# Performance work log

Measured on AMD Instinct MI355X. Metric: run time of the kernel, lower is better.

## Reference

```python
import jax, jax.numpy as jnp
import numpy as np

VOCAB, BLOCK, C, H, L = 65, 60, 384, 6, 6
HS = C // H  # 64
EPS = 1e-5


def _ln(x, g, b):
    mu = jnp.mean(x, axis=-1, keepdims=True)
    var = jnp.mean(jnp.square(x - mu), axis=-1, keepdims=True)
    return (x - mu) * jax.lax.rsqrt(var + EPS) * g + b


def setup_inputs() -> dict:
    key = jax.random.key(0)
    ks = jax.random.split(key, 16)
    std = 0.02
    B, T = 2048, 60
    inp = {
        'context': jax.random.randint(ks[0], (B, T), 0, VOCAB),
        'tok_emb': std * jax.random.normal(ks[1], (VOCAB, C), jnp.float32),
        'pos_emb': std * jax.random.normal(ks[2], (BLOCK, C), jnp.float32),
        # per-head projections stacked: [L, H, C, HS]
        'wq': std * jax.random.normal(ks[3], (L, H, C, HS), jnp.float32),
        'wk': std * jax.random.normal(ks[4], (L, H, C, HS), jnp.float32),
        'wv': std * jax.random.normal(ks[5], (L, H, C, HS), jnp.float32),
        'wo': std * jax.random.normal(ks[6], (L, C, C), jnp.float32),
        'bo': jnp.zeros((L, C), jnp.float32),
        'ln1_g': jnp.ones((L, C), jnp.float32),
        'ln1_b': jnp.zeros((L, C), jnp.float32),
        'ln2_g': jnp.ones((L, C), jnp.float32),
        'ln2_b': jnp.zeros((L, C), jnp.float32),
        'w1': std * jax.random.normal(ks[7], (L, C, 4 * C), jnp.float32),
        'b1': jnp.zeros((L, 4 * C), jnp.float32),
        'w2': std * jax.random.normal(ks[8], (L, 4 * C, C), jnp.float32),
        'b2': jnp.zeros((L, C), jnp.float32),
        'lnf_g': jnp.ones((C,), jnp.float32),
        'lnf_b': jnp.zeros((C,), jnp.float32),
        'lm_w': std * jax.random.normal(ks[9], (C, VOCAB), jnp.float32),
        'lm_b': jnp.zeros((VOCAB,), jnp.float32),
    }
    return inp


def _forward(context, tok_emb, pos_emb, wq, wk, wv, wo, bo,
             ln1_g, ln1_b, ln2_g, ln2_b, w1, b1, w2, b2,
             lnf_g, lnf_b, lm_w, lm_b):
    B, T = context.shape
    x = tok_emb[context] + pos_emb[:T]  # [B,T,C]
    causal = jnp.tril(jnp.ones((T, T), bool))
    neg_inf = jnp.finfo(x.dtype).min

    def block(x, p):
        (wq_l, wk_l, wv_l, wo_l, bo_l, g1, b1n, g2, b2n, w1_l, bb1, w2_l, bb2) = p
        h = _ln(x, g1, b1n)
        q = jnp.einsum('btc,hcd->bhtd', h, wq_l)
        k = jnp.einsum('btc,hcd->bhtd', h, wk_l)
        v = jnp.einsum('btc,hcd->bhtd', h, wv_l)
        scores = jnp.einsum('bhtd,bhsd->bhts', q, k) * (HS ** -0.5)
        scores = jnp.where(causal, scores, neg_inf)
        probs = jax.nn.softmax(scores, axis=-1)
        o = jnp.einsum('bhts,bhsd->bhtd', probs, v)
        o = o.transpose(0, 2, 1, 3).reshape(B, T, C)  # concat heads
        x = x + o @ wo_l + bo_l
        h = _ln(x, g2, b2n)
        x = x + jax.nn.relu(h @ w1_l + bb1) @ w2_l + bb2
        return x, None

    params = (wq, wk, wv, wo, bo, ln1_g, ln1_b, ln2_g, ln2_b, w1, b1, w2, b2)
    x, _ = jax.lax.scan(block, x, params)
    x = _ln(x, lnf_g, lnf_b)
    return x @ lm_w + lm_b  # [B,T,VOCAB]


def reference(context, tok_emb, pos_emb, wq, wk, wv, wo, bo,
              ln1_g, ln1_b, ln2_g, ln2_b, w1, b1, w2, b2,
              lnf_g, lnf_b, lm_w, lm_b):
    return _forward(context, tok_emb, pos_emb, wq, wk, wv, wo, bo,
                    ln1_g, ln1_b, ln2_g, ln2_b, w1, b1, w2, b2,
                    lnf_g, lnf_b, lm_w, lm_b)
```

## Files before the change

### kernel.cpp

```cpp
#include <hip/hip_runtime.h>


#define B_  2048
#define T_  60
#define C_  384
#define H_  6
#define HS_ 64
#define L_  6
#define FF_ 1536
#define V_  65

typedef unsigned int  u32;
typedef unsigned short u16;
typedef short bf16x8 __attribute__((ext_vector_type(8)));
typedef float f32x4  __attribute__((ext_vector_type(4)));

__device__ __forceinline__ float bf2f(u32 u) {
  return __uint_as_float(u << 16);
}
__device__ __forceinline__ u16 f2bf(float f) {
  u32 u = __float_as_uint(f);
  u = u + 0x7FFFu + ((u >> 16) & 1u);
  return (u16)(u >> 16);
}

__global__ void tconv_k(const float* __restrict__ src, u16* __restrict__ dst,
                        int K, int N, long srcStride, int nH, long sL, long sH)
{
  __shared__ float t[32][33];
  int z = blockIdx.z;
  int l = z / nH, hh = z % nH;
  const float* s = src + (long)z * srcStride;
  u16* d = dst + l * sL + hh * sH;
  int n0 = blockIdx.x * 32, k0 = blockIdx.y * 32;
  for (int yy = threadIdx.y; yy < 32; yy += 8) {
    int k = k0 + yy, n = n0 + threadIdx.x;
    t[yy][threadIdx.x] = (k < K && n < N) ? s[(long)k * N + n] : 0.f;
  }
  __syncthreads();
  for (int yy = threadIdx.y; yy < 32; yy += 8) {
    int n = n0 + yy, k = k0 + threadIdx.x;
    if (n < N && k < K) d[(long)n * K + k] = f2bf(t[threadIdx.x][yy]);
  }
}

__global__ __launch_bounds__(256) void embed_k(const int* __restrict__ ctx,
    const float* __restrict__ tok, const float* __restrict__ pos,
    float* __restrict__ x)
{
  int idx = blockIdx.x * 256 + threadIdx.x;
  int row = idx / (C_ / 4);
  int c   = (idx % (C_ / 4)) * 4;
  int t   = row % T_;
  int tk  = ctx[row];
  float4 a = *(const float4*)(tok + (long)tk * C_ + c);
  float4 p = *(const float4*)(pos + (long)t  * C_ + c);
  float4 o = make_float4(a.x + p.x, a.y + p.y, a.z + p.z, a.w + p.w);
  *(float4*)(x + (long)idx * 4) = o;
}

__global__ __launch_bounds__(256) void ln_k(const float* __restrict__ x,
    const float* __restrict__ g, const float* __restrict__ b,
    u16* __restrict__ h)
{
  int lane = threadIdx.x & 63;
  int wv   = threadIdx.x >> 6;
  long row = (long)blockIdx.x * 4 + wv;
  const float* xr = x + row * C_;
  int c0 = lane * 6;
  float v0[6];
  #pragma unroll
  for (int i = 0; i < 6; i++) v0[i] = xr[c0 + i];
  float s = 0.f, sq = 0.f;
  #pragma unroll
  for (int i = 0; i < 6; i++) { s += v0[i]; sq += v0[i] * v0[i]; }
  #pragma unroll
  for (int off = 32; off > 0; off >>= 1) {
    s  += __shfl_xor(s,  off, 64);
    sq += __shfl_xor(sq, off, 64);
  }
  float mu  = s * (1.f / C_);
  float var = sq * (1.f / C_) - mu * mu;
  float rs  = rsqrtf(var + 1e-5f);
  u16* hr = h + row * C_;
  #pragma unroll
  for (int i = 0; i < 6; i++) {
    float hv = (v0[i] - mu) * rs * g[c0 + i] + b[c0 + i];
    hr[c0 + i] = f2bf(hv);
  }
}

template<int RELU, int RES, int OBF>
__global__ __launch_bounds__(256) void gemm128d(const u16* __restrict__ A,
    const u16* __restrict__ Wt, const float* __restrict__ bias,
    const float* __restrict__ resid, void* __restrict__ outp,
    int N, int K, int mT, int nT)
{
  __shared__ __align__(16) u16 As[2][4][128][8];
  __shared__ __align__(16) u16 Bs[2][4][128][8];
  int tid = threadIdx.x;
  int bid = blockIdx.x;
  int mtile, ntile;
  if ((mT & 7) == 0) {
    int xcd = bid & 7, loc = bid >> 3;
    int q = loc / nT;
    mtile = xcd * (mT >> 3) + q;
    ntile = loc - q * nT;
  } else {
    int q = bid / nT;
    mtile = q;
    ntile = bid - q * nT;
  }
  long mBase = (long)mtile * 128;
  int  nBase = ntile * 128;
  int lane = tid & 63, wv = tid >> 6;
  int l15 = lane & 15, l4 = lane >> 4;
  int sk = tid & 3, sr = tid >> 2;
  const u16* aP = A + (mBase + sr) * (long)K + sk * 8;
  const u16* bP = Wt + ((long)nBase + sr) * K + sk * 8;
  const long rStep = (long)64 * K;

  f32x4 acc[2][8];
  #pragma unroll
  for (int i = 0; i < 2; i++)
    #pragma unroll
    for (int j = 0; j < 8; j++)
      acc[i][j] = (f32x4){0.f, 0.f, 0.f, 0.f};

  uint4 ar0 = *(const uint4*)aP;
  uint4 ar1 = *(const uint4*)(aP + rStep);
  uint4 br0 = *(const uint4*)bP;
  uint4 br1 = *(const uint4*)(bP + rStep);
  *(uint4*)&As[0][sk][sr][0]      = ar0;
  *(uint4*)&As[0][sk][sr + 64][0] = ar1;
  *(uint4*)&Bs[0][sk][sr][0]      = br0;
  *(uint4*)&Bs[0][sk][sr + 64][0] = br1;
  if (K > 32) {
    ar0 = *(const uint4*)(aP + 32);
    ar1 = *(const uint4*)(aP + rStep + 32);
    br0 = *(const uint4*)(bP + 32);
    br1 = *(const uint4*)(bP + rStep + 32);
  }
  __syncthreads();

  int cur = 0;
  for (int k0 = 0; k0 < K; k0 += 32) {
    bf16x8 af[2], bfr[8];
    af[0] = *(const bf16x8*)&As[cur][l4][wv * 32 + l15][0];
    af[1] = *(const bf16x8*)&As[cur][l4][wv * 32 + 16 + l15][0];
    #pragma unroll
    for (int j = 0; j < 8; j++)
      bfr[j] = *(const bf16x8*)&Bs[cur][l4][j * 16 + l15][0];
    if (k0 + 32 < K) {
      int nb = cur ^ 1;
      *(uint4*)&As[nb][sk][sr][0]      = ar0;
      *(uint4*)&As[nb][sk][sr + 64][0] = ar1;
      *(uint4*)&Bs[nb][sk][sr][0]      = br0;
      *(uint4*)&Bs[nb][sk][sr + 64][0] = br1;
      if (k0 + 64 < K) {
        ar0 = *(const uint4*)(aP + k0 + 64);
        ar1 = *(const uint4*)(aP + rStep + k0 + 64);
        br0 = *(const uint4*)(bP + k0 + 64);
        br1 = *(const uint4*)(bP + rStep + k0 + 64);
      }
    }
    #pragma unroll
    for (int i = 0; i < 2; i++)
      #pragma unroll
      for (int j = 0; j < 8; j++)
        acc[i][j] = __builtin_amdgcn_mfma_f32_16x16x32_bf16(
            af[i], bfr[j], acc[i][j], 0, 0, 0);
    __syncthreads();
    cur ^= 1;
  }

  #pragma unroll
  for (int i = 0; i < 2; i++) {
    #pragma unroll
    for (int j = 0; j < 8; j++) {
      int n = nBase + j * 16 + l15;
      float bv = bias ? bias[n] : 0.f;
      #pragma unroll
      for (int r = 0; r < 4; r++) {
        long row = mBase + wv * 32 + i * 16 + l4 * 4 + r;
        float vv = acc[i][j][r] + bv;
        if (RELU) vv = fmaxf(vv, 0.f);
        if (RES)  vv += resid[row * N + n];
        if (OBF) ((u16*)outp)[row * N + n] = f2bf(vv);
        else     ((float*)outp)[row * N + n] = vv;
      }
    }
  }
}

template<int OBF>
__global__ __launch_bounds__(256) void gemm_head(const u16* __restrict__ A,
    const u16* __restrict__ Wt, const float* __restrict__ bias,
    void* __restrict__ outp, int N, int K)
{
  __shared__ __align__(16) u16 As[4][128][8];
  __shared__ __align__(16) u16 Bs[4][64][8];
  int tid  = threadIdx.x;
  int nt   = blockIdx.x;
  int nBase = nt * 64;
  long mBase = (long)blockIdx.y * 128;
  int lane = tid & 63, wv = tid >> 6;
  int l15 = lane & 15, l4 = lane >> 4;
  int sseg = tid & 3;
  int srow = tid >> 2;
  const u16* a0p = A + (mBase + srow) * K + sseg * 8;
  const u16* a1p = a0p + (long)64 * K;
  bool colOK = (nBase + srow) < N;
  const u16* bp  = Wt + (long)(nBase + srow) * K + sseg * 8;

  f32x4 acc[2][4];
  #pragma unroll
  for (int i = 0; i < 2; i++)
    #pragma unroll
    for (int j = 0; j < 4; j++)
      acc[i][j] = (f32x4){0.f, 0.f, 0.f, 0.f};

  for (int k0 = 0; k0 < K; k0 += 32) {
    uint4 av0 = *(const uint4*)(a0p + k0);
    uint4 av1 = *(const uint4*)(a1p + k0);
    uint4 bv  = colOK ? *(const uint4*)(bp + k0) : make_uint4(0, 0, 0, 0);
    *(uint4*)&As[sseg][srow][0]      = av0;
    *(uint4*)&As[sseg][srow + 64][0] = av1;
    *(uint4*)&Bs[sseg][srow][0]      = bv;
    __syncthreads();
    bf16x8 af[2], bfr[4];
    af[0] = *(const bf16x8*)&As[l4][wv * 32 + l15][0];
    af[1] = *(const bf16x8*)&As[l4][wv * 32 + 16 + l15][0];
    #pragma unroll
    for (int j = 0; j < 4; j++)
      bfr[j] = *(const bf16x8*)&Bs[l4][j * 16 + l15][0];
    #pragma unroll
    for (int i = 0; i < 2; i++)
      #pragma unroll
      for (int j = 0; j < 4; j++)
        acc[i][j] = __builtin_amdgcn_mfma_f32_16x16x32_bf16(
            af[i], bfr[j], acc[i][j], 0, 0, 0);
    __syncthreads();
  }

  #pragma unroll
  for (int i = 0; i < 2; i++) {
    #pragma unroll
    for (int j = 0; j < 4; j++) {
      int n = nBase + j * 16 + l15;
      if (n < N) {
        #pragma unroll
        for (int r = 0; r < 4; r++) {
          long row = mBase + wv * 32 + i * 16 + l4 * 4 + r;
          float vv = acc[i][j][r];
          if (bias) vv += bias[n];
          if (OBF) ((u16*)outp)[row * N + n] = f2bf(vv);
          else     ((float*)outp)[row * N + n] = vv;
        }
      }
    }
  }
}

__global__ __launch_bounds__(256) void attn_k(const u16* __restrict__ qkv,
    u16* __restrict__ ao)
{
  __shared__ __align__(16) u16 qs[64][72];
  __shared__ __align__(16) u16 ks[64][72];
  __shared__ __align__(16) u16 vT[64][72];
  __shared__ __align__(16) u16 ps[64][72];
  int tid = threadIdx.x;
  int bb = blockIdx.x / H_;
  int hh = blockIdx.x % H_;
  const u16* base = qkv + ((long)bb * T_) * 1152 + hh * HS_;

  for (int i = tid; i < 576; i += 256)
    ((uint4*)vT)[i] = make_uint4(0, 0, 0, 0);
  __syncthreads();

  for (int i = tid; i < 480; i += 256) {
    int t = i >> 3, d0 = (i & 7) << 3;
    const u16* rp = base + (long)t * 1152;
    *(uint4*)&qs[t][d0] = *(const uint4*)(rp + d0);
    *(uint4*)&ks[t][d0] = *(const uint4*)(rp + 384 + d0);
    uint4 rv = *(const uint4*)(rp + 768 + d0);
    u16 vv[8] = {(u16)(rv.x & 0xffffu), (u16)(rv.x >> 16),
                 (u16)(rv.y & 0xffffu), (u16)(rv.y >> 16),
                 (u16)(rv.z & 0xffffu), (u16)(rv.z >> 16),
                 (u16)(rv.w & 0xffffu), (u16)(rv.w >> 16)};
    #pragma unroll
    for (int m = 0; m < 8; m++) vT[d0 + m][t] = vv[m];
  }
  __syncthreads();

  int lane = tid & 63, wv = tid >> 6;
  int l15 = lane & 15, quad = lane >> 4;

  bf16x8 aq0 = *(const bf16x8*)&qs[wv * 16 + l15][quad * 8];
  bf16x8 aq1 = *(const bf16x8*)&qs[wv * 16 + l15][32 + quad * 8];
  f32x4 s[4];
  #pragma unroll
  for (int jt = 0; jt < 4; jt++) {
    bf16x8 b0 = *(const bf16x8*)&ks[jt * 16 + l15][quad * 8];
    bf16x8 b1 = *(const bf16x8*)&ks[jt * 16 + l15][32 + quad * 8];
    f32x4 a2 = (f32x4){0.f, 0.f, 0.f, 0.f};
    a2 = __builtin_amdgcn_mfma_f32_16x16x32_bf16(aq0, b0, a2, 0, 0, 0);
    a2 = __builtin_amdgcn_mfma_f32_16x16x32_bf16(aq1, b1, a2, 0, 0, 0);
    s[jt] = a2;
  }

  int rbase = wv * 16 + quad * 4;
  #pragma unroll
  for (int r = 0; r < 4; r++) {
    int row = rbase + r;
    float v0[4];
    #pragma unroll
    for (int jt = 0; jt < 4; jt++) {
      int col = jt * 16 + l15;
      float sv = s[jt][r] * 0.125f;
      v0[jt] = (col <= row) ? sv : -1e30f;
    }
    float m = fmaxf(fmaxf(v0[0], v0[1]), fmaxf(v0[2], v0[3]));
    #pragma unroll
    for (int off = 1; off < 16; off <<= 1) m = fmaxf(m, __shfl_xor(m, off, 64));
    float sum = 0.f;
    #pragma unroll
    for (int jt = 0; jt < 4; jt++) { v0[jt] = __expf(v0[jt] - m); sum += v0[jt]; }
    #pragma unroll
    for (int off = 1; off < 16; off <<= 1) sum += __shfl_xor(sum, off, 64);
    float inv = 1.f / sum;
    #pragma unroll
    for (int jt = 0; jt < 4; jt++)
      ps[row][jt * 16 + l15] = f2bf(v0[jt] * inv);
  }
  __syncthreads();

  bf16x8 ap0 = *(const bf16x8*)&ps[wv * 16 + l15][quad * 8];
  bf16x8 ap1 = *(const bf16x8*)&ps[wv * 16 + l15][32 + quad * 8];
  long obase = ((long)bb * T_) * C_ + hh * HS_;
  #pragma unroll
  for (int dt = 0; dt < 4; dt++) {
    bf16x8 b0 = *(const bf16x8*)&vT[dt * 16 + l15][quad * 8];
    bf16x8 b1 = *(const bf16x8*)&vT[dt * 16 + l15][32 + quad * 8];
    f32x4 a2 = (f32x4){0.f, 0.f, 0.f, 0.f};
    a2 = __builtin_amdgcn_mfma_f32_16x16x32_bf16(ap0, b0, a2, 0, 0, 0);
    a2 = __builtin_amdgcn_mfma_f32_16x16x32_bf16(ap1, b1, a2, 0, 0, 0);
    #pragma unroll
    for (int r = 0; r < 4; r++) {
      int row = rbase + r;
      if (row < T_)
        ao[obase + (long)row * C_ + dt * 16 + l15] = f2bf(a2[r]);
    }
  }
}

extern "C" void kernel_launch(void* const* d_in, const int* in_sizes, int n_in,
                              void* d_out, int out_size, void* d_ws, size_t ws_size,
                              hipStream_t stream)
{
  const int*   ctx  = (const int*)  d_in[0];
  const float* tok  = (const float*)d_in[1];
  const float* pos  = (const float*)d_in[2];
  const float* wq   = (const float*)d_in[3];
  const float* wk   = (const float*)d_in[4];
  const float* wv   = (const float*)d_in[5];
  const float* wo   = (const float*)d_in[6];
  const float* bo   = (const float*)d_in[7];
  const float* ln1g = (const float*)d_in[8];
  const float* ln1b = (const float*)d_in[9];
  const float* ln2g = (const float*)d_in[10];
  const float* ln2b = (const float*)d_in[11];
  const float* w1   = (const float*)d_in[12];
  const float* b1   = (const float*)d_in[13];
  const float* w2   = (const float*)d_in[14];
  const float* b2   = (const float*)d_in[15];
  const float* lnfg = (const float*)d_in[16];
  const float* lnfb = (const float*)d_in[17];
  const float* lmw  = (const float*)d_in[18];
  const float* lmb  = (const float*)d_in[19];
  float* out = (float*)d_out;

  const long nQKV = (long)L_ * H_ * C_ * HS_;
  const long nWO  = (long)L_ * C_ * C_;
  const long nW1  = (long)L_ * C_ * FF_;
  const long nLM  = (long)C_ * V_;
  u16* wqkvT = (u16*)d_ws;
  u16* woT = wqkvT + 3 * nQKV;
  u16* w1T = woT + nWO;
  u16* w2T = w1T + nW1;
  u16* lmT = w2T + nW1;
  const size_t wbytes = (size_t)(nQKV * 3 + nWO + nW1 * 2 + nLM) * 2;

  int chunkB = 32;
  {
    const int cand[] = {2048, 1024, 512, 256, 128, 64, 32};
    for (int i = 0; i < 7; i++) {
      size_t U = (size_t)cand[i] * T_ * C_ * 2;
      if (wbytes + 7 * U <= ws_size) { chunkB = cand[i]; break; }
    }
  }
  const long BTc = (long)chunkB * T_;
  char* wsb = (char*)d_ws + wbytes;
  const size_t U = (size_t)BTc * C_ * 2;
  float* x    = (float*)wsb;
  u16*   h    = (u16*)(wsb + 2 * U);
  char*  reg  = wsb + 3 * U;
  u16* qkvb = (u16*)reg;
  u16* ab   = (u16*)(reg + 3 * U);
  u16* fb   = (u16*)reg;

  {
    dim3 tb(32, 8);
    const long sL = 1152L * 384, sH = 64L * 384, sec = 384L * 384;
    tconv_k<<<dim3(2, 12, L_ * H_), tb, 0, stream>>>(wq, wqkvT,
        C_, HS_, (long)C_ * HS_, H_, sL, sH);
    tconv_k<<<dim3(2, 12, L_ * H_), tb, 0, stream>>>(wk, wqkvT + sec,
        C_, HS_, (long)C_ * HS_, H_, sL, sH);
    tconv_k<<<dim3(2, 12, L_ * H_), tb, 0, stream>>>(wv, wqkvT + 2 * sec,
        C_, HS_, (long)C_ * HS_, H_, sL, sH);
    tconv_k<<<dim3(12, 12, L_), tb, 0, stream>>>(wo, woT,
        C_, C_, (long)C_ * C_, 1, (long)C_ * C_, 0);
    tconv_k<<<dim3(48, 12, L_), tb, 0, stream>>>(w1, w1T,
        C_, FF_, (long)C_ * FF_, 1, (long)C_ * FF_, 0);
    tconv_k<<<dim3(12, 48, L_), tb, 0, stream>>>(w2, w2T,
        FF_, C_, (long)FF_ * C_, 1, (long)FF_ * C_, 0);
    tconv_k<<<dim3(3, 12, 1), tb, 0, stream>>>(lmw, lmT,
        C_, V_, (long)C_ * V_, 1, 0, 0);
  }

  const long qkvL = 1152L * 384;
  const long woL  = (long)C_ * C_;
  const long w1L  = (long)C_ * FF_;
  dim3 blk(256);
  dim3 gEmb((u32)(BTc * C_ / 4 / 256));
  dim3 gLN((u32)(BTc / 4));
  int mT = (int)(BTc / 128);
  dim3 gHd(2, (u32)(BTc / 128));
  dim3 gAt((u32)(chunkB * H_));

  for (int c0 = 0; c0 < B_; c0 += chunkB) {
    const long tok0 = (long)c0 * T_;
    const int* ctxc = ctx + tok0;
    float* outc = out + tok0 * V_;

    embed_k<<<gEmb, blk, 0, stream>>>(ctxc, tok, pos, x);

    for (int l = 0; l < L_; l++) {
      ln_k<<<gLN, blk, 0, stream>>>(x, ln1g + l * C_, ln1b + l * C_, h);
      gemm128d<0,0,1><<<dim3(mT * 9), blk, 0, stream>>>(h, wqkvT + l * qkvL,
          nullptr, nullptr, qkvb, 1152, C_, mT, 9);
      attn_k<<<gAt, blk, 0, stream>>>(qkvb, ab);
      gemm128d<0,1,0><<<dim3(mT * 3), blk, 0, stream>>>(ab, woT + l * woL,
          bo + l * C_, x, x, C_, C_, mT, 3);
      ln_k<<<gLN, blk, 0, stream>>>(x, ln2g + l * C_, ln2b + l * C_, h);
      gemm128d<1,0,1><<<dim3(mT * 12), blk, 0, stream>>>(h, w1T + l * w1L,
          b1 + l * FF_, nullptr, fb, FF_, C_, mT, 12);
      gemm128d<0,1,0><<<dim3(mT * 3), blk, 0, stream>>>(fb, w2T + l * w1L,
          b2 + l * C_, x, x, C_, FF_, mT, 3);
    }

    ln_k<<<gLN, blk, 0, stream>>>(x, lnfg, lnfb, h);
    gemm_head<0><<<gHd, blk, 0, stream>>>(h, lmT, lmb, outc, V_, C_);
  }
}
```

Before: 5.966 ms.

## Use 2x2 wave tiling and XOR-swizzled row-major LDS layout in GEMM kernels

```diff
diff --git a/kernel.cpp b/kernel.cpp
--- a/kernel.cpp
+++ b/kernel.cpp
@@ -96,8 +96,8 @@
     const float* __restrict__ resid, void* __restrict__ outp,
     int N, int K, int mT, int nT)
 {
-  __shared__ __align__(16) u16 As[2][4][128][8];
-  __shared__ __align__(16) u16 Bs[2][4][128][8];
+  __shared__ __align__(16) u16 As[2][128][4][8];
+  __shared__ __align__(16) u16 Bs[2][128][4][8];
   int tid = threadIdx.x;
   int bid = blockIdx.x;
   int mtile, ntile;
@@ -115,26 +115,29 @@
   int  nBase = ntile * 128;
   int lane = tid & 63, wv = tid >> 6;
   int l15 = lane & 15, l4 = lane >> 4;
+  int wr = wv >> 1, wc = wv & 1;
   int sk = tid & 3, sr = tid >> 2;
+  int swW = sk ^ ((sr >> 2) & 3);
+  int swR = l4 ^ (l15 >> 2);
   const u16* aP = A + (mBase + sr) * (long)K + sk * 8;
   const u16* bP = Wt + ((long)nBase + sr) * K + sk * 8;
   const long rStep = (long)64 * K;
 
-  f32x4 acc[2][8];
-  #pragma unroll
-  for (int i = 0; i < 2; i++)
-    #pragma unroll
-    for (int j = 0; j < 8; j++)
+  f32x4 acc[4][4];
+  #pragma unroll
+  for (int i = 0; i < 4; i++)
+    #pragma unroll
+    for (int j = 0; j < 4; j++)
       acc[i][j] = (f32x4){0.f, 0.f, 0.f, 0.f};
 
   uint4 ar0 = *(const uint4*)aP;
   uint4 ar1 = *(const uint4*)(aP + rStep);
   uint4 br0 = *(const uint4*)bP;
   uint4 br1 = *(const uint4*)(bP + rStep);
-  *(uint4*)&As[0][sk][sr][0]      = ar0;
-  *(uint4*)&As[0][sk][sr + 64][0] = ar1;
-  *(uint4*)&Bs[0][sk][sr][0]      = br0;
-  *(uint4*)&Bs[0][sk][sr + 64][0] = br1;
+  *(uint4*)&As[0][sr][swW][0]      = ar0;
+  *(uint4*)&As[0][sr + 64][swW][0] = ar1;
+  *(uint4*)&Bs[0][sr][swW][0]      = br0;
+  *(uint4*)&Bs[0][sr + 64][swW][0] = br1;
   if (K > 32) {
     ar0 = *(const uint4*)(aP + 32);
     ar1 = *(const uint4*)(aP + rStep + 32);
@@ -145,18 +148,19 @@
 
   int cur = 0;
   for (int k0 = 0; k0 < K; k0 += 32) {
-    bf16x8 af[2], bfr[8];
-    af[0] = *(const bf16x8*)&As[cur][l4][wv * 32 + l15][0];
-    af[1] = *(const bf16x8*)&As[cur][l4][wv * 32 + 16 + l15][0];
-    #pragma unroll
-    for (int j = 0; j < 8; j++)
-      bfr[j] = *(const bf16x8*)&Bs[cur][l4][j * 16 + l15][0];
+    bf16x8 af[4], bfr[4];
+    #pragma unroll
+    for (int i = 0; i < 4; i++)
+      af[i] = *(const bf16x8*)&As[cur][wr * 64 + i * 16 + l15][swR][0];
+    #pragma unroll
+    for (int j = 0; j < 4; j++)
+      bfr[j] = *(const bf16x8*)&Bs[cur][wc * 64 + j * 16 + l15][swR][0];
     if (k0 + 32 < K) {
       int nb = cur ^ 1;
-      *(uint4*)&As[nb][sk][sr][0]      = ar0;
-      *(uint4*)&As[nb][sk][sr + 64][0] = ar1;
-      *(uint4*)&Bs[nb][sk][sr][0]      = br0;
-      *(uint4*)&Bs[nb][sk][sr + 64][0] = br1;
+      *(uint4*)&As[nb][sr][swW][0]      = ar0;
+      *(uint4*)&As[nb][sr + 64][swW][0] = ar1;
+      *(uint4*)&Bs[nb][sr][swW][0]      = br0;
+      *(uint4*)&Bs[nb][sr + 64][swW][0] = br1;
       if (k0 + 64 < K) {
         ar0 = *(const uint4*)(aP + k0 + 64);
         ar1 = *(const uint4*)(aP + rStep + k0 + 64);
@@ -165,9 +169,9 @@
       }
     }
     #pragma unroll
-    for (int i = 0; i < 2; i++)
+    for (int i = 0; i < 4; i++)
       #pragma unroll
-      for (int j = 0; j < 8; j++)
+      for (int j = 0; j < 4; j++)
         acc[i][j] = __builtin_amdgcn_mfma_f32_16x16x32_bf16(
             af[i], bfr[j], acc[i][j], 0, 0, 0);
     __syncthreads();
@@ -175,14 +179,14 @@
   }
 
   #pragma unroll
-  for (int i = 0; i < 2; i++) {
-    #pragma unroll
-    for (int j = 0; j < 8; j++) {
-      int n = nBase + j * 16 + l15;
+  for (int i = 0; i < 4; i++) {
+    #pragma unroll
+    for (int j = 0; j < 4; j++) {
+      int n = nBase + wc * 64 + j * 16 + l15;
       float bv = bias ? bias[n] : 0.f;
       #pragma unroll
       for (int r = 0; r < 4; r++) {
-        long row = mBase + wv * 32 + i * 16 + l4 * 4 + r;
+        long row = mBase + wr * 64 + i * 16 + l4 * 4 + r;
         float vv = acc[i][j][r] + bv;
         if (RELU) vv = fmaxf(vv, 0.f);
         if (RES)  vv += resid[row * N + n];
@@ -198,8 +202,8 @@
     const u16* __restrict__ Wt, const float* __restrict__ bias,
     void* __restrict__ outp, int N, int K)
 {
-  __shared__ __align__(16) u16 As[4][128][8];
-  __shared__ __align__(16) u16 Bs[4][64][8];
+  __shared__ __align__(16) u16 As[128][4][8];
+  __shared__ __align__(16) u16 Bs[64][4][8];
   int tid  = threadIdx.x;
   int nt   = blockIdx.x;
   int nBase = nt * 64;
@@ -208,6 +212,8 @@
   int l15 = lane & 15, l4 = lane >> 4;
   int sseg = tid & 3;
   int srow = tid >> 2;
+  int swW = sseg ^ ((srow >> 2) & 3);
+  int swR = l4 ^ (l15 >> 2);
   const u16* a0p = A + (mBase + srow) * K + sseg * 8;
   const u16* a1p = a0p + (long)64 * K;
   bool colOK = (nBase + srow) < N;
@@ -224,16 +230,16 @@
     uint4 av0 = *(const uint4*)(a0p + k0);
     uint4 av1 = *(const uint4*)(a1p + k0);
     uint4 bv  = colOK ? *(const uint4*)(bp + k0) : make_uint4(0, 0, 0, 0);
-    *(uint4*)&As[sseg][srow][0]      = av0;
-    *(uint4*)&As[sseg][srow + 64][0] = av1;
-    *(uint4*)&Bs[sseg][srow][0]      = bv;
+    *(uint4*)&As[srow][swW][0]      = av0;
+    *(uint4*)&As[srow + 64][swW][0] = av1;
+    *(uint4*)&Bs[srow][swW][0]      = bv;
     __syncthreads();
     bf16x8 af[2], bfr[4];
-    af[0] = *(const bf16x8*)&As[l4][wv * 32 + l15][0];
-    af[1] = *(const bf16x8*)&As[l4][wv * 32 + 16 + l15][0];
+    af[0] = *(const bf16x8*)&As[wv * 32 + l15][swR][0];
+    af[1] = *(const bf16x8*)&As[wv * 32 + 16 + l15][swR][0];
     #pragma unroll
     for (int j = 0; j < 4; j++)
-      bfr[j] = *(const bf16x8*)&Bs[l4][j * 16 + l15][0];
+      bfr[j] = *(const bf16x8*)&Bs[j * 16 + l15][swR][0];
     #pragma unroll
     for (int i = 0; i < 2; i++)
       #pragma unroll
```

Result: faster. 5.821 ms (-2.4%).
